# Kernel tuning notes

Hardware: AMD Instinct MI355X
Metric: run time of the kernel (lower is better)

Reference implementation:

```python
import jax, jax.numpy as jnp
import numpy as np


def setup_inputs() -> dict:
    key = jax.random.key(0)
    ks = jax.random.split(key, 8)
    N, E, F, H = 50000, 400000, 128, 512
    x = jax.random.normal(ks[0], (N, F), dtype=jnp.float32)
    edge_index = jax.random.randint(ks[1], (2, E), 0, N, dtype=jnp.int32)
    W1 = jax.random.normal(ks[2], (H, 2 * F), dtype=jnp.float32) * 0.05
    b1 = jax.random.normal(ks[3], (H,), dtype=jnp.float32) * 0.05
    W2 = jax.random.normal(ks[4], (H, 2 * H), dtype=jnp.float32) * 0.05
    b2 = jax.random.normal(ks[5], (H,), dtype=jnp.float32) * 0.05
    Wo = jax.random.normal(ks[6], (1, H), dtype=jnp.float32) * 0.05
    bo = jax.random.normal(ks[7], (1,), dtype=jnp.float32) * 0.05
    return {"x": x, "edge_index": edge_index, "W1": W1, "b1": b1,
            "W2": W2, "b2": b2, "Wo": Wo, "bo": bo}


def reference(x, edge_index, W1, b1, W2, b2, Wo, bo):
    # GraphSAGE mean aggregation: agg[dst] = mean over incoming edges of h[src]
    N = x.shape[0]
    src = edge_index[0]
    dst = edge_index[1]
    deg = jax.ops.segment_sum(jnp.ones_like(dst, dtype=x.dtype), dst,
                              num_segments=N)
    inv_deg = 1.0 / jnp.maximum(deg, 1.0)  # clamp_min(1.0)

    def agg_mean(h):
        s = jax.ops.segment_sum(h[src], dst, num_segments=N)  # [N, D]
        return s * inv_deg[:, None]

    # Layer 1: concat(self, neigh) -> Linear -> ReLU (dropout = identity, eval)
    n1 = agg_mean(x)
    h1 = jax.nn.relu(jnp.concatenate([x, n1], axis=1) @ W1.T + b1)
    # Layer 2
    n2 = agg_mean(h1)
    h2 = jax.nn.relu(jnp.concatenate([h1, n2], axis=1) @ W2.T + b2)
    # Output head
    logits = h2 @ Wo.T + bo  # [N, 1]
    return jax.nn.sigmoid(logits)
```

## Files before the change

kernel.cpp:

```cpp
#include <hip/hip_runtime.h>
#include <math.h>


typedef __attribute__((ext_vector_type(8))) short bf16x8;
typedef __attribute__((ext_vector_type(4))) float f32x4;

static inline int ceil_div(int a, int b) { return (a + b - 1) / b; }

__device__ inline float bf2f_lo(unsigned u) { return __builtin_bit_cast(float, u << 16); }
__device__ inline float bf2f_hi(unsigned u) { return __builtin_bit_cast(float, u & 0xffff0000u); }
__device__ inline unsigned f2bf(float f) {
    unsigned u = __builtin_bit_cast(unsigned, f);
    u += 0x7fffu + ((u >> 16) & 1u);
    return u >> 16;
}

#define GLOAD_LDS16(gp, lp)                                                   \
    __builtin_amdgcn_global_load_lds(                                         \
        (__attribute__((address_space(1))) void*)(gp),                        \
        (__attribute__((address_space(3))) void*)(lp), 16, 0, 0)


__global__ void cvt3_hist_kernel(const float* __restrict__ a, unsigned short* __restrict__ ao, int na4,
                                 const float* __restrict__ b, unsigned short* __restrict__ bo, int nb4,
                                 const float* __restrict__ c, unsigned short* __restrict__ co, int nc4,
                                 const int* __restrict__ dst, int* __restrict__ deg, int E,
                                 int cvt_blocks) {
    if ((int)blockIdx.x < cvt_blocks) {
        int i = blockIdx.x * 256 + threadIdx.x;
        if (i < na4) {
            float4 v = ((const float4*)a)[i];
            ushort4 o;
            o.x = (unsigned short)f2bf(v.x);
            o.y = (unsigned short)f2bf(v.y);
            o.z = (unsigned short)f2bf(v.z);
            o.w = (unsigned short)f2bf(v.w);
            ((ushort4*)ao)[i] = o;
        } else if (i < na4 + nb4) {
            int kk = i - na4;
            float4 v = ((const float4*)b)[kk];
            ushort4 o;
            o.x = (unsigned short)f2bf(v.x);
            o.y = (unsigned short)f2bf(v.y);
            o.z = (unsigned short)f2bf(v.z);
            o.w = (unsigned short)f2bf(v.w);
            const int cc = kk >> 6;
            const int kq = kk & 63;
            const int t    = kq >> 3;
            const int quad = (kq >> 1) & 3;
            const int j0   = (kq & 1) * 4;
            const int g  = cc >> 6, nt = (cc >> 4) & 3, cl = cc & 15;
            const size_t off =
                ((((size_t)(t * 8 + g) * 4 + nt) * 4 + quad) * 16 + cl) * 8 + j0;
            *(ushort4*)(bo + off) = o;
        } else if (i < na4 + nb4 + nc4) {
            int kk = i - na4 - nb4;
            float4 v = ((const float4*)c)[kk];
            ushort4 o;
            o.x = (unsigned short)f2bf(v.x);
            o.y = (unsigned short)f2bf(v.y);
            o.z = (unsigned short)f2bf(v.z);
            o.w = (unsigned short)f2bf(v.w);
            const int cc = kk >> 8;
            const int kq = kk & 255;
            const int t    = kq >> 3;
            const int quad = (kq >> 1) & 3;
            const int j0   = (kq & 1) * 4;
            const int g  = cc >> 6, nt = (cc >> 4) & 3, cl = cc & 15;
            const size_t off =
                ((((size_t)(t * 8 + g) * 4 + nt) * 4 + quad) * 16 + cl) * 8 + j0;
            *(ushort4*)(co + off) = o;
        }
    } else {
        int e = (blockIdx.x - cvt_blocks) * 256 + threadIdx.x;
        if (e < E) atomicAdd(&deg[dst[e]], 1);
    }
}


__global__ __launch_bounds__(256) void chunk_reduce(const int* __restrict__ deg,
                                                    int* __restrict__ partial, int N) {
    int base = blockIdx.x * 1024;
    int s = 0;
    for (int i = threadIdx.x; i < 1024; i += 256) {
        int idx = base + i;
        if (idx < N) s += deg[idx];
    }
    #pragma unroll
    for (int off = 32; off; off >>= 1) s += __shfl_down(s, off);
    __shared__ int ws[4];
    if ((threadIdx.x & 63) == 0) ws[threadIdx.x >> 6] = s;
    __syncthreads();
    if (threadIdx.x == 0) partial[blockIdx.x] = ws[0] + ws[1] + ws[2] + ws[3];
}

__global__ void partial_scan(int* __restrict__ partial, int* __restrict__ rowstartN, int P) {
    int lane = threadIdx.x;
    int v = (lane < P) ? partial[lane] : 0;
    int incl = v;
    #pragma unroll
    for (int off = 1; off < 64; off <<= 1) {
        int t = __shfl_up(incl, off);
        if (lane >= off) incl += t;
    }
    if (lane < P) partial[lane] = incl - v;
    if (lane == 63) *rowstartN = incl;
}

__global__ __launch_bounds__(256) void chunk_scan(const int* __restrict__ deg,
                                                  const int* __restrict__ partial,
                                                  int* __restrict__ rowstart,
                                                  int* __restrict__ cursor, int N) {
    int base = blockIdx.x * 1024 + threadIdx.x * 4;
    int v[4];
    #pragma unroll
    for (int j = 0; j < 4; ++j) {
        int i = base + j;
        v[j] = (i < N) ? deg[i] : 0;
    }
    int mysum = v[0] + v[1] + v[2] + v[3];
    int incl = mysum;
    int lane = threadIdx.x & 63, wave = threadIdx.x >> 6;
    #pragma unroll
    for (int off = 1; off < 64; off <<= 1) {
        int t = __shfl_up(incl, off);
        if (lane >= off) incl += t;
    }
    __shared__ int ws[4];
    if (lane == 63) ws[wave] = incl;
    __syncthreads();
    int run = partial[blockIdx.x] + incl - mysum;
    for (int w = 0; w < wave; ++w) run += ws[w];
    #pragma unroll
    for (int j = 0; j < 4; ++j) {
        int i = base + j;
        if (i < N) { rowstart[i] = run; cursor[i] = run; }
        run += v[j];
    }
}

__global__ void bucket_kernel(const int* __restrict__ src, const int* __restrict__ dst,
                              int* __restrict__ cursor, int* __restrict__ ebuf, int E) {
    int e = blockIdx.x * 256 + threadIdx.x;
    if (e < E) {
        int pos = atomicAdd(&cursor[dst[e]], 1);
        ebuf[pos] = src[e];
    }
}


__global__ void gather_mean_128(const int* __restrict__ rowstart, const int* __restrict__ ebuf,
                                const unsigned* __restrict__ featb, unsigned* __restrict__ outb, int N) {
    int w = (blockIdx.x * blockDim.x + threadIdx.x) >> 6;
    int lane = threadIdx.x & 63;
    if (w >= N) return;
    int e0 = rowstart[w], e1 = rowstart[w + 1];
    float ax = 0.0f, ay = 0.0f;
    for (int i = e0; i < e1; i += 8) {
        int idx[8];
        #pragma unroll
        for (int u = 0; u < 8; ++u) {
            int t = i + u;
            idx[u] = ebuf[t < e1 ? t : e1 - 1];
        }
        unsigned v[8];
        #pragma unroll
        for (int u = 0; u < 8; ++u)
            v[u] = featb[(size_t)idx[u] * 64 + lane];
        #pragma unroll
        for (int u = 0; u < 8; ++u) {
            const float s = (i + u < e1) ? 1.0f : 0.0f;
            ax += s * bf2f_lo(v[u]);
            ay += s * bf2f_hi(v[u]);
        }
    }
    float inv = 1.0f / fmaxf((float)(e1 - e0), 1.0f);
    outb[(size_t)w * 64 + lane] = f2bf(ax * inv) | (f2bf(ay * inv) << 16);
}

__global__ void gather_mean_512(const int* __restrict__ rowstart, const int* __restrict__ ebuf,
                                const unsigned short* __restrict__ featb,
                                unsigned short* __restrict__ outb, int N) {
    int w = (blockIdx.x * blockDim.x + threadIdx.x) >> 6;
    int lane = threadIdx.x & 63;
    if (w >= N) return;
    int e0 = rowstart[w], e1 = rowstart[w + 1];
    float a[8] = {0, 0, 0, 0, 0, 0, 0, 0};
    const uint4* base = (const uint4*)featb;
    for (int i = e0; i < e1; i += 8) {
        int idx[8];
        #pragma unroll
        for (int u = 0; u < 8; ++u) {
            int t = i + u;
            idx[u] = ebuf[t < e1 ? t : e1 - 1];
        }
        uint4 v[8];
        #pragma unroll
        for (int u = 0; u < 8; ++u)
            v[u] = base[(size_t)idx[u] * 64 + lane];
        #pragma unroll
        for (int u = 0; u < 8; ++u) {
            const float s = (i + u < e1) ? 1.0f : 0.0f;
            a[0] += s * bf2f_lo(v[u].x); a[1] += s * bf2f_hi(v[u].x);
            a[2] += s * bf2f_lo(v[u].y); a[3] += s * bf2f_hi(v[u].y);
            a[4] += s * bf2f_lo(v[u].z); a[5] += s * bf2f_hi(v[u].z);
            a[6] += s * bf2f_lo(v[u].w); a[7] += s * bf2f_hi(v[u].w);
        }
    }
    float inv = 1.0f / fmaxf((float)(e1 - e0), 1.0f);
    uint4 o;
    o.x = f2bf(a[0] * inv) | (f2bf(a[1] * inv) << 16);
    o.y = f2bf(a[2] * inv) | (f2bf(a[3] * inv) << 16);
    o.z = f2bf(a[4] * inv) | (f2bf(a[5] * inv) << 16);
    o.w = f2bf(a[6] * inv) | (f2bf(a[7] * inv) << 16);
    ((uint4*)outb)[(size_t)w * 64 + lane] = o;
}


#define STGAg(kt, SPL, STR) do {                                               \
    const unsigned short* _p = ((kt) < (SPL)) ? (A0 + ((kt) << 5))             \
                                              : (A1 + (((kt) - (SPL)) << 5));  \
    GLOAD_LDS16(_p + offA, lds + ((kt) % 3) * 8192 + w * 1024);                \
} while (0)

#define LDBg(kt, bqr) do {                                                     \
    _Pragma("unroll")                                                          \
    for (int _n = 0; _n < 4; ++_n)                                             \
        bqr[_n] = *(const bf16x8*)(W +                                         \
            (((size_t)(kt) * 8 + gB) * 4 + _n) * 512 + l * 8);                 \
} while (0)

#define RDAg(bf) do {                                                         \
    _Pragma("unroll")                                                          \
    for (int _m = 0; _m < 4; ++_m)                                             \
        af[_m] = *(const bf16x8*)(lds + (bf) * 8192 + aoff + _m * 1024);       \
} while (0)

#define MMg(bqr) do {                                                          \
    _Pragma("unroll")                                                          \
    for (int _m = 0; _m < 4; ++_m)                                             \
        _Pragma("unroll")                                                      \
        for (int _n = 0; _n < 4; ++_n)                                         \
            acc[_m][_n] = __builtin_amdgcn_mfma_f32_16x16x32_bf16(             \
                af[_m], bqr[_n], acc[_m][_n], 0, 0, 0);                        \
} while (0)

#define PHASEg(t, stg, bqr, gstr, SPL, STR) do {                               \
    __builtin_amdgcn_sched_barrier(0);                                         \
    asm volatile("s_waitcnt vmcnt(" gstr ")" ::: "memory");                    \
    __builtin_amdgcn_s_barrier();                                              \
    __builtin_amdgcn_sched_barrier(0);                                         \
    RDAg((t) % 3);                                                             \
    if (stg) STGAg((t) + 2, SPL, STR);                                         \
    __builtin_amdgcn_s_setprio(1);                                             \
    MMg(bqr);                                                                  \
    __builtin_amdgcn_s_setprio(0);                                             \
    if (stg) LDBg((t) + 2, bqr);                                               \
} while (0)

#define BREG_PRELUDE(STR)                                                      \
    const int nwg  = ((N + 127) >> 7) * 2;                                     \
    const int orig = blockIdx.x;                                               \
    const int xcd = orig & 7, lnum = orig >> 3;                                \
    const int q = nwg >> 3, r = nwg & 7;                                       \
    const int virt = (xcd < r ? xcd * (q + 1)                                  \
                              : r * (q + 1) + (xcd - r) * q) + lnum;           \
    const int row0 = (virt >> 1) << 7;                                         \
    const int col0 = (virt & 1) << 8;                                          \
    const int tid = threadIdx.x;                                               \
    const int w = tid >> 6, l = tid & 63;                                      \
    const int wr = w >> 2, wc = w & 3;                                         \
    const int cl = l & 15, quad = l >> 4;                                      \
    const int gB = (col0 >> 6) + wc;                                           \
    const int c_log = (((l & 3) ^ ((l >> 3) & 3))) * 8;                        \
    int ra = row0 + w * 16 + (l >> 2);                                         \
    if (ra > N - 1) ra = N - 1;                                                \
    const size_t offA = (size_t)ra * (STR) + c_log;                            \
    const int swz  = ((cl >> 1) & 3) << 4;                                     \
    const int aoff = (((wr * 64 + cl) * 64) + quad * 16) ^ swz;                \
    f32x4 acc[4][4];                                                           \
    _Pragma("unroll")                                                          \
    for (int mt = 0; mt < 4; ++mt)                                             \
        _Pragma("unroll")                                                      \
        for (int nt = 0; nt < 4; ++nt)                                         \
            acc[mt][nt] = (f32x4){0.f, 0.f, 0.f, 0.f};                         \
    bf16x8 af[4], bqA[4], bqB[4];                                              \
    (void)wr;

__global__ __launch_bounds__(512, 4) void gemm1_breg(
    const unsigned short* __restrict__ A0,
    const unsigned short* __restrict__ A1,
    const unsigned short* __restrict__ W,
    const float* __restrict__ b,
    unsigned short* __restrict__ outb,
    int N)
{
    __shared__ char lds[24576];
    BREG_PRELUDE(128)

    STGAg(0, 4, 128); LDBg(0, bqA);
    STGAg(1, 4, 128); LDBg(1, bqB);

    #pragma unroll
    for (int t = 0; t < 6; t += 2) {
        PHASEg(t,     1, bqA, "5", 4, 128);
        PHASEg(t + 1, 1, bqB, "5", 4, 128);
    }
    PHASEg(6, 0, bqA, "5", 4, 128);
    PHASEg(7, 0, bqB, "0", 4, 128);

    #pragma unroll
    for (int nt = 0; nt < 4; ++nt) {
        const int colx = col0 + wc * 64 + nt * 16 + cl;
        const float bb = b[colx];
        #pragma unroll
        for (int mt = 0; mt < 4; ++mt) {
            #pragma unroll
            for (int rr = 0; rr < 4; ++rr) {
                const int row = row0 + wr * 64 + mt * 16 + quad * 4 + rr;
                if (row < N)
                    outb[(size_t)row * 512 + colx] =
                        (unsigned short)f2bf(fmaxf(acc[mt][nt][rr] + bb, 0.0f));
            }
        }
    }
}

__global__ __launch_bounds__(512, 4) void gemm2_breg(
    const unsigned short* __restrict__ A0,
    const unsigned short* __restrict__ A1,
    const unsigned short* __restrict__ W,
    const float* __restrict__ b,
    const float* __restrict__ Wo,
    float* __restrict__ logit,
    int N)
{
    __shared__ char lds[24576];
    BREG_PRELUDE(512)

    STGAg(0, 16, 512); LDBg(0, bqA);
    STGAg(1, 16, 512); LDBg(1, bqB);

    #pragma unroll
    for (int t = 0; t < 30; t += 2) {
        PHASEg(t,     1, bqA, "5", 16, 512);
        PHASEg(t + 1, 1, bqB, "5", 16, 512);
    }
    PHASEg(30, 0, bqA, "5", 16, 512);
    PHASEg(31, 0, bqB, "0", 16, 512);

    float bv[4], wv[4];
    #pragma unroll
    for (int nt = 0; nt < 4; ++nt) {
        const int colx = col0 + wc * 64 + nt * 16 + cl;
        bv[nt] = b[colx];
        wv[nt] = Wo[colx];
    }
    #pragma unroll
    for (int mt = 0; mt < 4; ++mt) {
        #pragma unroll
        for (int rr = 0; rr < 4; ++rr) {
            float s = 0.0f;
            #pragma unroll
            for (int nt = 0; nt < 4; ++nt)
                s += fmaxf(acc[mt][nt][rr] + bv[nt], 0.0f) * wv[nt];
            s += __shfl_xor(s, 1);
            s += __shfl_xor(s, 2);
            s += __shfl_xor(s, 4);
            s += __shfl_xor(s, 8);
            const int row = row0 + wr * 64 + mt * 16 + quad * 4 + rr;
            if (cl == 0 && row < N) atomicAdd(&logit[row], s);
        }
    }
}

__global__ void head_kernel(const float* __restrict__ logit, const float* __restrict__ bo,
                            float* __restrict__ out, int N) {
    int i = blockIdx.x * 256 + threadIdx.x;
    if (i < N) out[i] = 1.0f / (1.0f + expf(-(logit[i] + bo[0])));
}

extern "C" void kernel_launch(void* const* d_in, const int* in_sizes, int n_in,
                              void* d_out, int out_size, void* d_ws, size_t ws_size,
                              hipStream_t stream) {
    const float* x  = (const float*)d_in[0];
    const int*   ei = (const int*)d_in[1];
    const float* W1 = (const float*)d_in[2];
    const float* b1 = (const float*)d_in[3];
    const float* W2 = (const float*)d_in[4];
    const float* b2 = (const float*)d_in[5];
    const float* Wo = (const float*)d_in[6];
    const float* bo = (const float*)d_in[7];
    float* out = (float*)d_out;

    const int N = in_sizes[0] / 128;
    const int E = in_sizes[1] / 2;
    const int* src = ei;
    const int* dst = ei + E;

    char* ws = (char*)d_ws;
    size_t off = 0;
    auto alloc = [&](size_t bytes) {
        void* p = ws + off;
        off += (bytes + 255) & ~(size_t)255;
        return p;
    };
    int* deg      = (int*)alloc((size_t)N * 4);
    int* rowstart = (int*)alloc((size_t)(N + 1) * 4);
    int* cursor   = (int*)alloc((size_t)N * 4);
    int* partial  = (int*)alloc((size_t)64 * 4);
    int* ebuf     = (int*)alloc((size_t)E * 4);
    float* logit  = (float*)alloc((size_t)N * 4);
    unsigned short* xb  = (unsigned short*)alloc((size_t)N * 128 * 2);
    unsigned short* W1b = (unsigned short*)alloc((size_t)512 * 256 * 2);
    unsigned short* W2b = (unsigned short*)alloc((size_t)512 * 1024 * 2);
    unsigned short* n1b = (unsigned short*)alloc((size_t)N * 128 * 2);
    unsigned short* h1b = (unsigned short*)alloc((size_t)N * 512 * 2);
    unsigned short* n2b = (unsigned short*)alloc((size_t)N * 512 * 2);
    (void)ws_size; (void)n_in; (void)out_size;

    hipMemsetAsync(deg,   0, (size_t)N * 4, stream);
    hipMemsetAsync(logit, 0, (size_t)N * 4, stream);

    const int na4 = N * 128 / 4, nb4 = 512 * 256 / 4, nc4 = 512 * 1024 / 4;
    const int cvt_blocks  = ceil_div(na4 + nb4 + nc4, 256);
    const int hist_blocks = ceil_div(E, 256);
    cvt3_hist_kernel<<<cvt_blocks + hist_blocks, 256, 0, stream>>>(
        x, xb, na4, W1, W1b, nb4, W2, W2b, nc4, dst, deg, E, cvt_blocks);

    const int P = ceil_div(N, 1024);
    chunk_reduce<<<P, 256, 0, stream>>>(deg, partial, N);
    partial_scan<<<1, 64, 0, stream>>>(partial, rowstart + N, P);
    chunk_scan<<<P, 256, 0, stream>>>(deg, partial, rowstart, cursor, N);
    bucket_kernel<<<ceil_div(E, 256), 256, 0, stream>>>(src, dst, cursor, ebuf, E);

    const int g2 = ceil_div(N, 128) * 2;

    gather_mean_128<<<ceil_div(N * 64, 256), 256, 0, stream>>>(rowstart, ebuf,
                                                               (const unsigned*)xb, (unsigned*)n1b, N);
    gemm1_breg<<<g2, 512, 0, stream>>>(xb, n1b, W1b, b1, h1b, N);

    gather_mean_512<<<ceil_div(N * 64, 256), 256, 0, stream>>>(rowstart, ebuf, h1b, n2b, N);
    gemm2_breg<<<g2, 512, 0, stream>>>(h1b, n2b, W2b, b2, Wo, logit, N);

    head_kernel<<<ceil_div(N, 256), 256, 0, stream>>>(logit, bo, out, N);
}
```

Measured before the change: 316.4 us.

## Retile GEMMs to 64x512 per block, fuse head into GEMM2, merge scan kernels

```diff
diff --git a/kernel.cpp b/kernel.cpp
--- a/kernel.cpp
+++ b/kernel.cpp
@@ -94,42 +94,46 @@
     if (threadIdx.x == 0) partial[blockIdx.x] = ws[0] + ws[1] + ws[2] + ws[3];
 }
 
-__global__ void partial_scan(int* __restrict__ partial, int* __restrict__ rowstartN, int P) {
-    int lane = threadIdx.x;
-    int v = (lane < P) ? partial[lane] : 0;
-    int incl = v;
+__global__ __launch_bounds__(256) void chunk_scan(const int* __restrict__ deg,
+                                                  const int* __restrict__ partial,
+                                                  int* __restrict__ rowstart,
+                                                  int* __restrict__ cursor, int N, int P) {
+    __shared__ int off_sh;
+    __shared__ int ws[4];
+    if (threadIdx.x < 64) {
+        const int j = threadIdx.x;
+        const int pv = (j < P) ? partial[j] : 0;
+        int tot = pv;
+        #pragma unroll
+        for (int o = 1; o < 64; o <<= 1) tot += __shfl_xor(tot, o);
+        int mv = (j < (int)blockIdx.x) ? pv : 0;
+        #pragma unroll
+        for (int o = 1; o < 64; o <<= 1) mv += __shfl_xor(mv, o);
+        if (j == 0) {
+            off_sh = mv;
+            if (blockIdx.x == 0) rowstart[N] = tot;
+        }
+    }
+    __syncthreads();
+
+    int base = blockIdx.x * 1024 + threadIdx.x * 4;
+    int v[4];
+    #pragma unroll
+    for (int j = 0; j < 4; ++j) {
+        int i = base + j;
+        v[j] = (i < N) ? deg[i] : 0;
+    }
+    int mysum = v[0] + v[1] + v[2] + v[3];
+    int incl = mysum;
+    int lane = threadIdx.x & 63, wave = threadIdx.x >> 6;
     #pragma unroll
     for (int off = 1; off < 64; off <<= 1) {
         int t = __shfl_up(incl, off);
         if (lane >= off) incl += t;
     }
-    if (lane < P) partial[lane] = incl - v;
-    if (lane == 63) *rowstartN = incl;
-}
-
-__global__ __launch_bounds__(256) void chunk_scan(const int* __restrict__ deg,
-                                                  const int* __restrict__ partial,
-                                                  int* __restrict__ rowstart,
-                                                  int* __restrict__ cursor, int N) {
-    int base = blockIdx.x * 1024 + threadIdx.x * 4;
-    int v[4];
-    #pragma unroll
-    for (int j = 0; j < 4; ++j) {
-        int i = base + j;
-        v[j] = (i < N) ? deg[i] : 0;
-    }
-    int mysum = v[0] + v[1] + v[2] + v[3];
-    int incl = mysum;
-    int lane = threadIdx.x & 63, wave = threadIdx.x >> 6;
-    #pragma unroll
-    for (int off = 1; off < 64; off <<= 1) {
-        int t = __shfl_up(incl, off);
-        if (lane >= off) incl += t;
-    }
-    __shared__ int ws[4];
     if (lane == 63) ws[wave] = incl;
     __syncthreads();
-    int run = partial[blockIdx.x] + incl - mysum;
+    int run = off_sh + incl - mysum;
     for (int w = 0; w < wave; ++w) run += ws[w];
     #pragma unroll
     for (int j = 0; j < 4; ++j) {
@@ -217,10 +221,11 @@
 }
 
 
-#define STGAg(kt, SPL, STR) do {                                               \
-    const unsigned short* _p = ((kt) < (SPL)) ? (A0 + ((kt) << 5))             \
-                                              : (A1 + (((kt) - (SPL)) << 5));  \
-    GLOAD_LDS16(_p + offA, lds + ((kt) % 3) * 8192 + w * 1024);                \
+#define STGP(kt, SPL) do {                                                     \
+    const int _ktw = (kt) + (w >> 2);                                          \
+    const unsigned short* _p = (_ktw < (SPL))                                  \
+        ? (A0 + (_ktw << 5)) : (A1 + ((_ktw - (SPL)) << 5));                   \
+    GLOAD_LDS16(_p + offA, lds + (((kt) >> 1) % 3) * 8192 + w * 1024);         \
 } while (0)
 
 #define LDBg(kt, bqr) do {                                                     \
@@ -230,10 +235,11 @@
             (((size_t)(kt) * 8 + gB) * 4 + _n) * 512 + l * 8);                 \
 } while (0)
 
-#define RDAg(bf) do {                                                         \
+#define RDAp(p) do {                                                           \
     _Pragma("unroll")                                                          \
     for (int _m = 0; _m < 4; ++_m)                                             \
-        af[_m] = *(const bf16x8*)(lds + (bf) * 8192 + aoff + _m * 1024);       \
+        af[_m] = *(const bf16x8*)(lds + (((p) >> 1) % 3) * 8192 +              \
+                  ((p) & 1) * 4096 + aoff + _m * 1024);                        \
 } while (0)
 
 #define MMg(bqr) do {                                                          \
@@ -245,47 +251,44 @@
                 af[_m], bqr[_n], acc[_m][_n], 0, 0, 0);                        \
 } while (0)
 
-#define PHASEg(t, stg, bqr, gstr, SPL, STR) do {                               \
+#define PH(p, bqr, gs, stg, ldb, SPL) do {                                     \
     __builtin_amdgcn_sched_barrier(0);                                         \
-    asm volatile("s_waitcnt vmcnt(" gstr ")" ::: "memory");                    \
+    asm volatile("s_waitcnt vmcnt(" gs ")" ::: "memory");                      \
     __builtin_amdgcn_s_barrier();                                              \
     __builtin_amdgcn_sched_barrier(0);                                         \
-    RDAg((t) % 3);                                                             \
-    if (stg) STGAg((t) + 2, SPL, STR);                                         \
+    RDAp(p);                                                                   \
     __builtin_amdgcn_s_setprio(1);                                             \
     MMg(bqr);                                                                  \
     __builtin_amdgcn_s_setprio(0);                                             \
-    if (stg) LDBg((t) + 2, bqr);                                               \
+    if (ldb) LDBg((p) + 2, bqr);                                               \
+    if (stg) STGP((p) + 4, SPL);                                               \
 } while (0)
 
 #define BREG_PRELUDE(STR)                                                      \
-    const int nwg  = ((N + 127) >> 7) * 2;                                     \
+    const int nwg  = (N + 63) >> 6;                                            \
     const int orig = blockIdx.x;                                               \
     const int xcd = orig & 7, lnum = orig >> 3;                                \
     const int q = nwg >> 3, r = nwg & 7;                                       \
     const int virt = (xcd < r ? xcd * (q + 1)                                  \
                               : r * (q + 1) + (xcd - r) * q) + lnum;           \
-    const int row0 = (virt >> 1) << 7;                                         \
-    const int col0 = (virt & 1) << 8;                                          \
+    const int row0 = virt << 6;                                                \
     const int tid = threadIdx.x;                                               \
     const int w = tid >> 6, l = tid & 63;                                      \
-    const int wr = w >> 2, wc = w & 3;                                         \
     const int cl = l & 15, quad = l >> 4;                                      \
-    const int gB = (col0 >> 6) + wc;                                           \
+    const int gB = w;                                                          \
     const int c_log = (((l & 3) ^ ((l >> 3) & 3))) * 8;                        \
-    int ra = row0 + w * 16 + (l >> 2);                                         \
+    int ra = row0 + (w & 3) * 16 + (l >> 2);                                   \
     if (ra > N - 1) ra = N - 1;                                                \
     const size_t offA = (size_t)ra * (STR) + c_log;                            \
     const int swz  = ((cl >> 1) & 3) << 4;                                     \
-    const int aoff = (((wr * 64 + cl) * 64) + quad * 16) ^ swz;                \
+    const int aoff = (cl * 64 + quad * 16) ^ swz;                              \
     f32x4 acc[4][4];                                                           \
     _Pragma("unroll")                                                          \
     for (int mt = 0; mt < 4; ++mt)                                             \
         _Pragma("unroll")                                                      \
         for (int nt = 0; nt < 4; ++nt)                                         \
             acc[mt][nt] = (f32x4){0.f, 0.f, 0.f, 0.f};                         \
-    bf16x8 af[4], bqA[4], bqB[4];                                              \
-    (void)wr;
+    bf16x8 af[4], bqA[4], bqB[4];
 
 __global__ __launch_bounds__(512, 4) void gemm1_breg(
     const unsigned short* __restrict__ A0,
@@ -298,26 +301,27 @@
     __shared__ char lds[24576];
     BREG_PRELUDE(128)
 
-    STGAg(0, 4, 128); LDBg(0, bqA);
-    STGAg(1, 4, 128); LDBg(1, bqB);
-
-    #pragma unroll
-    for (int t = 0; t < 6; t += 2) {
-        PHASEg(t,     1, bqA, "5", 4, 128);
-        PHASEg(t + 1, 1, bqB, "5", 4, 128);
-    }
-    PHASEg(6, 0, bqA, "5", 4, 128);
-    PHASEg(7, 0, bqB, "0", 4, 128);
+    STGP(0, 4); LDBg(0, bqA);
+    STGP(2, 4); LDBg(1, bqB);
+
+    PH(0, bqA, "5", 1, 1, 4);
+    PH(1, bqB, "5", 0, 1, 4);
+    PH(2, bqA, "4", 1, 1, 4);
+    PH(3, bqB, "5", 0, 1, 4);
+    PH(4, bqA, "4", 0, 1, 4);
+    PH(5, bqB, "4", 0, 1, 4);
+    PH(6, bqA, "4", 0, 0, 4);
+    PH(7, bqB, "0", 0, 0, 4);
 
     #pragma unroll
     for (int nt = 0; nt < 4; ++nt) {
-        const int colx = col0 + wc * 64 + nt * 16 + cl;
+        const int colx = w * 64 + nt * 16 + cl;
         const float bb = b[colx];
         #pragma unroll
         for (int mt = 0; mt < 4; ++mt) {
             #pragma unroll
             for (int rr = 0; rr < 4; ++rr) {
-                const int row = row0 + wr * 64 + mt * 16 + quad * 4 + rr;
+                const int row = row0 + mt * 16 + quad * 4 + rr;
                 if (row < N)
                     outb[(size_t)row * 512 + colx] =
                         (unsigned short)f2bf(fmaxf(acc[mt][nt][rr] + bb, 0.0f));
@@ -332,30 +336,36 @@
     const unsigned short* __restrict__ W,
     const float* __restrict__ b,
     const float* __restrict__ Wo,
-    float* __restrict__ logit,
+    const float* __restrict__ bo,
+    float* __restrict__ out,
     int N)
 {
     __shared__ char lds[24576];
     BREG_PRELUDE(512)
 
-    STGAg(0, 16, 512); LDBg(0, bqA);
-    STGAg(1, 16, 512); LDBg(1, bqB);
-
-    #pragma unroll
-    for (int t = 0; t < 30; t += 2) {
-        PHASEg(t,     1, bqA, "5", 16, 512);
-        PHASEg(t + 1, 1, bqB, "5", 16, 512);
-    }
-    PHASEg(30, 0, bqA, "5", 16, 512);
-    PHASEg(31, 0, bqB, "0", 16, 512);
+    STGP(0, 16); LDBg(0, bqA);
+    STGP(2, 16); LDBg(1, bqB);
+
+    PH(0, bqA, "5", 1, 1, 16);
+    PH(1, bqB, "5", 0, 1, 16);
+    #pragma unroll
+    for (int p = 2; p < 28; p += 2) {
+        PH(p,     bqA, "4", (p <= 26), 1, 16);
+        PH(p + 1, bqB, "5", 0,         1, 16);
+    }
+    PH(28, bqA, "4", 0, 1, 16);
+    PH(29, bqB, "4", 0, 1, 16);
+    PH(30, bqA, "4", 0, 0, 16);
+    PH(31, bqB, "0", 0, 0, 16);
 
     float bv[4], wv[4];
     #pragma unroll
     for (int nt = 0; nt < 4; ++nt) {
-        const int colx = col0 + wc * 64 + nt * 16 + cl;
+        const int colx = w * 64 + nt * 16 + cl;
         bv[nt] = b[colx];
         wv[nt] = Wo[colx];
     }
+    float* ls = (float*)lds;
     #pragma unroll
     for (int mt = 0; mt < 4; ++mt) {
         #pragma unroll
@@ -368,16 +378,17 @@
             s += __shfl_xor(s, 2);
             s += __shfl_xor(s, 4);
             s += __shfl_xor(s, 8);
-            const int row = row0 + wr * 64 + mt * 16 + quad * 4 + rr;
-            if (cl == 0 && row < N) atomicAdd(&logit[row], s);
-        }
-    }
-}
-
-__global__ void head_kernel(const float* __restrict__ logit, const float* __restrict__ bo,
-                            float* __restrict__ out, int N) {
-    int i = blockIdx.x * 256 + threadIdx.x;
-    if (i < N) out[i] = 1.0f / (1.0f + expf(-(logit[i] + bo[0])));
+            if (cl == 0) ls[(mt * 16 + quad * 4 + rr) * 8 + w] = s;
+        }
+    }
+    __syncthreads();
+    if (tid < 64) {
+        float s = 0.0f;
+        #pragma unroll
+        for (int w8 = 0; w8 < 8; ++w8) s += ls[tid * 8 + w8];
+        const int row = row0 + tid;
+        if (row < N) out[row] = 1.0f / (1.0f + expf(-(s + bo[0])));
+    }
 }
 
 extern "C" void kernel_launch(void* const* d_in, const int* in_sizes, int n_in,
@@ -410,7 +421,6 @@
     int* cursor   = (int*)alloc((size_t)N * 4);
     int* partial  = (int*)alloc((size_t)64 * 4);
     int* ebuf     = (int*)alloc((size_t)E * 4);
-    float* logit  = (float*)alloc((size_t)N * 4);
     unsigned short* xb  = (unsigned short*)alloc((size_t)N * 128 * 2);
     unsigned short* W1b = (unsigned short*)alloc((size_t)512 * 256 * 2);
     unsigned short* W2b = (unsigned short*)alloc((size_t)512 * 1024 * 2);
@@ -419,8 +429,7 @@
     unsigned short* n2b = (unsigned short*)alloc((size_t)N * 512 * 2);
     (void)ws_size; (void)n_in; (void)out_size;
 
-    hipMemsetAsync(deg,   0, (size_t)N * 4, stream);
-    hipMemsetAsync(logit, 0, (size_t)N * 4, stream);
+    hipMemsetAsync(deg, 0, (size_t)N * 4, stream);
 
     const int na4 = N * 128 / 4, nb4 = 512 * 256 / 4, nc4 = 512 * 1024 / 4;
     const int cvt_blocks  = ceil_div(na4 + nb4 + nc4, 256);
@@ -430,18 +439,15 @@
 
     const int P = ceil_div(N, 1024);
     chunk_reduce<<<P, 256, 0, stream>>>(deg, partial, N);
-    partial_scan<<<1, 64, 0, stream>>>(partial, rowstart + N, P);
-    chunk_scan<<<P, 256, 0, stream>>>(deg, partial, rowstart, cursor, N);
+    chunk_scan<<<P, 256, 0, stream>>>(deg, partial, rowstart, cursor, N, P);
     bucket_kernel<<<ceil_div(E, 256), 256, 0, stream>>>(src, dst, cursor, ebuf, E);
 
-    const int g2 = ceil_div(N, 128) * 2;
+    const int g2 = ceil_div(N, 64);
 
     gather_mean_128<<<ceil_div(N * 64, 256), 256, 0, stream>>>(rowstart, ebuf,
                                                                (const unsigned*)xb, (unsigned*)n1b, N);
     gemm1_breg<<<g2, 512, 0, stream>>>(xb, n1b, W1b, b1, h1b, N);
 
     gather_mean_512<<<ceil_div(N * 64, 256), 256, 0, stream>>>(rowstart, ebuf, h1b, n2b, N);
-    gemm2_breg<<<g2, 512, 0, stream>>>(h1b, n2b, W2b, b2, Wo, logit, N);
-
-    head_kernel<<<ceil_div(N, 256), 256, 0, stream>>>(logit, bo, out, N);
-}
+    gemm2_breg<<<g2, 512, 0, stream>>>(h1b, n2b, W2b, b2, Wo, bo, out, N);
+}
```

Measured after the change: 310.0 us. -2.0%, faster.
